# Kernel tuning notes

Hardware: AMD Instinct MI355X
Metric: run time of the kernel (lower is better)

## Reference

```python
import jax, jax.numpy as jnp
import numpy as np

B, S, H = 4, 512, 128

def setup_inputs() -> dict:
    key = jax.random.key(0)
    ks = jax.random.split(key, 6)
    scale = 1.0 / np.sqrt(2 * H)
    return {
        "query": jax.random.normal(ks[0], (B, S, H), dtype=jnp.float32),
        "key": jax.random.normal(ks[1], (B, S, H), dtype=jnp.float32),
        "value": jax.random.normal(ks[2], (B, S, H), dtype=jnp.float32),
        "attn_W": jax.random.normal(ks[3], (H, 2 * H), dtype=jnp.float32) * scale,  # torch Linear weight [out=H, in=2H]
        "attn_b": jax.random.normal(ks[4], (H,), dtype=jnp.float32) * scale,
        "v_w": jax.random.normal(ks[5], (1, H), dtype=jnp.float32) * (1.0 / np.sqrt(H)),
    }

def reference(query, key, value, attn_W, attn_b, v_w):
    # Split the concat-linear into query/key halves: cat([q,k]) @ W.T == q @ Wq.T + k @ Wk.T
    Wq = attn_W[:, :H]  # [H, H]
    Wk = attn_W[:, H:]  # [H, H]
    q_proj = jnp.einsum('bsh,oh->bso', query, Wq) + attn_b  # [B,S,H]
    k_proj = jnp.einsum('bth,oh->bto', key, Wk)             # [B,S,H]
    # tanh(q_proj[:, :, None] + k_proj[:, None, :]) -> [B,S,S,H]
    hidden = jnp.tanh(q_proj[:, :, None, :] + k_proj[:, None, :, :])
    scores = jnp.einsum('bsth,h->bst', hidden, v_w[0])      # [B,S,S]
    attention_weights = jax.nn.softmax(scores, axis=-1)
    # dropout is identity in eval mode
    output = jnp.einsum('bst,bth->bsh', attention_weights, value)
    return output, attention_weights
```

## Files before the change

### kernel.cpp

```cpp
#include <hip/hip_runtime.h>

#define Bn 4
#define Sn 512
#define Hn 128
#define ST 4

__device__ __forceinline__ float fast_exp2(float x) { return __builtin_amdgcn_exp2f(x); }
__device__ __forceinline__ float fast_rcp(float x)  { return __builtin_amdgcn_rcpf(x); }

#define C2 2.8853900817779268f

__global__ __launch_bounds__(256) void proj_kernel(
    const float* __restrict__ query, const float* __restrict__ key,
    const float* __restrict__ attn_W, const float* __restrict__ attn_b,
    float* __restrict__ eq, float* __restrict__ ekT)
{
    __shared__ float rows[2][4][Hn];
    const int row0 = blockIdx.x * 4;
    const int b    = row0 / Sn;
    const int t0   = row0 % Sn;
    const int tid  = threadIdx.x;

    {
        int src = tid >> 7, r = (tid >> 5) & 3, c4 = tid & 31;
        ((float4*)rows)[tid] =
            reinterpret_cast<const float4*>(src ? key : query)[(row0 + r) * 32 + c4];
    }
    __syncthreads();

    const int o     = tid & 127;
    const int which = tid >> 7;
    float acc[4] = {0,0,0,0};
    const float* wrow = attn_W + o * (2 * Hn) + which * Hn;
    for (int c = 0; c < Hn; c += 4) {
        float4 wv = *reinterpret_cast<const float4*>(wrow + c);
        #pragma unroll
        for (int r = 0; r < 4; r++) {
            float4 rv = *reinterpret_cast<const float4*>(&rows[which][r][c]);
            acc[r] += rv.x * wv.x + rv.y * wv.y + rv.z * wv.z + rv.w * wv.w;
        }
    }
    if (which == 0) {
        float bias = attn_b[o];
        #pragma unroll
        for (int r = 0; r < 4; r++)
            eq[(row0 + r) * Hn + o] = fast_exp2(C2 * (acc[r] + bias));
    } else {
        float4 ev;
        ev.x = fast_exp2(C2 * acc[0]); ev.y = fast_exp2(C2 * acc[1]);
        ev.z = fast_exp2(C2 * acc[2]); ev.w = fast_exp2(C2 * acc[3]);
        *reinterpret_cast<float4*>(&ekT[(size_t)(b * Hn + o) * Sn + t0]) = ev;
    }
}

__global__ __launch_bounds__(256) void score_kernel(
    const float* __restrict__ eq, const float* __restrict__ ekT,
    const float* __restrict__ v_w, float* __restrict__ logits)
{
    const int b  = blockIdx.y;
    const int s  = blockIdx.x * ST + (threadIdx.x >> 6);
    const int t0 = blockIdx.z * 256 + (threadIdx.x & 63) * 4;

    const float* kb   = ekT + (size_t)b * Hn * Sn + t0;
    const float* qrow = eq + (size_t)(b * Sn + s) * Hn;

    float a0 = 0.f, a1 = 0.f, a2 = 0.f, a3 = 0.f;
    for (int h = 0; h < Hn; h += 8) {
        float4 qA = *reinterpret_cast<const float4*>(qrow + h);
        float4 qB = *reinterpret_cast<const float4*>(qrow + h + 4);
        float4 wA = *reinterpret_cast<const float4*>(v_w + h);
        float4 wB = *reinterpret_cast<const float4*>(v_w + h + 4);
        const float qj[8] = {qA.x, qA.y, qA.z, qA.w, qB.x, qB.y, qB.z, qB.w};
        const float wj[8] = {wA.x, wA.y, wA.z, wA.w, wB.x, wB.y, wB.z, wB.w};
        #pragma unroll
        for (int j = 0; j < 8; j++) {
            float4 e = *reinterpret_cast<const float4*>(kb + (size_t)(h + j) * Sn);
            const float q = qj[j], w = wj[j];
            a0 += w * fast_rcp(q * e.x + 1.0f);
            a1 += w * fast_rcp(q * e.y + 1.0f);
            a2 += w * fast_rcp(q * e.z + 1.0f);
            a3 += w * fast_rcp(q * e.w + 1.0f);
        }
    }
    float4 o;
    o.x = -2.0f * a0; o.y = -2.0f * a1; o.z = -2.0f * a2; o.w = -2.0f * a3;
    *reinterpret_cast<float4*>(logits + (size_t)(b * Sn + s) * Sn + t0) = o;
}

__global__ __launch_bounds__(512) void softpv_kernel(
    const float* __restrict__ value, float* __restrict__ out,
    float* __restrict__ out_w)
{
    __shared__ float4 scT4[Sn];
    __shared__ float4 part4[16][ST][Hn / 4];

    const int b   = blockIdx.y;
    const int s0  = blockIdx.x * ST;
    const int tid = threadIdx.x;
    const int wave = tid >> 6, lane = tid & 63;

    if (wave < ST) {
        const int sr = wave;
        float* row = out_w + (size_t)(b * Sn + s0 + sr) * Sn;
        float v[8]; float m = -1e30f;
        #pragma unroll
        for (int i = 0; i < 8; i++) { v[i] = row[lane + i * 64]; m = fmaxf(m, v[i]); }
        #pragma unroll
        for (int off = 32; off; off >>= 1) m = fmaxf(m, __shfl_xor(m, off, 64));
        float sum = 0.f;
        const float l2e = 1.4426950408889634f;
        #pragma unroll
        for (int i = 0; i < 8; i++) { v[i] = fast_exp2((v[i] - m) * l2e); sum += v[i]; }
        #pragma unroll
        for (int off = 32; off; off >>= 1) sum += __shfl_xor(sum, off, 64);
        float inv = 1.0f / sum;
        #pragma unroll
        for (int i = 0; i < 8; i++) {
            float wgt = v[i] * inv;
            row[lane + i * 64] = wgt;
            ((float*)&scT4[lane + i * 64])[sr] = wgt;
        }
    }
    __syncthreads();

    {
        const int hq = tid & 31, tg = tid >> 5;
        const float* vb = value + ((size_t)b * Sn + tg * 32) * Hn + hq * 4;
        float4 A0 = {0,0,0,0}, A1 = {0,0,0,0}, A2 = {0,0,0,0}, A3 = {0,0,0,0};
        #pragma unroll 4
        for (int i = 0; i < 32; i++) {
            float4 v4 = *reinterpret_cast<const float4*>(vb + i * Hn);
            float4 w4 = scT4[tg * 32 + i];
            A0.x += w4.x * v4.x; A0.y += w4.x * v4.y; A0.z += w4.x * v4.z; A0.w += w4.x * v4.w;
            A1.x += w4.y * v4.x; A1.y += w4.y * v4.y; A1.z += w4.y * v4.z; A1.w += w4.y * v4.w;
            A2.x += w4.z * v4.x; A2.y += w4.z * v4.y; A2.z += w4.z * v4.z; A2.w += w4.z * v4.w;
            A3.x += w4.w * v4.x; A3.y += w4.w * v4.y; A3.z += w4.w * v4.z; A3.w += w4.w * v4.w;
        }
        part4[tg][0][hq] = A0;
        part4[tg][1][hq] = A1;
        part4[tg][2][hq] = A2;
        part4[tg][3][hq] = A3;
    }
    __syncthreads();
    {
        const int sg = tid >> 7, h = tid & 127;
        float r = 0.f;
        #pragma unroll
        for (int tg = 0; tg < 16; tg++)
            r += ((const float*)&part4[tg][sg][h >> 2])[h & 3];
        out[(b * Sn + s0 + sg) * Hn + h] = r;
    }
}

extern "C" void kernel_launch(void* const* d_in, const int* in_sizes, int n_in,
                              void* d_out, int out_size, void* d_ws, size_t ws_size,
                              hipStream_t stream) {
    const float* query  = (const float*)d_in[0];
    const float* key    = (const float*)d_in[1];
    const float* value  = (const float*)d_in[2];
    const float* attn_W = (const float*)d_in[3];
    const float* attn_b = (const float*)d_in[4];
    const float* v_w    = (const float*)d_in[5];

    float* out   = (float*)d_out;
    float* out_w = out + Bn * Sn * Hn;

    float* eq  = (float*)d_ws;
    float* ekT = eq + Bn * Sn * Hn;

    proj_kernel<<<Bn * Sn / 4, 256, 0, stream>>>(query, key, attn_W, attn_b, eq, ekT);
    score_kernel<<<dim3(Sn / ST, Bn, 2), 256, 0, stream>>>(eq, ekT, v_w, out_w);
    softpv_kernel<<<dim3(Sn / ST, Bn), 512, 0, stream>>>(value, out, out_w);
}
```

Baseline: 45.31 us.

## Register-tile score kernel over 4x4 outputs and split hidden dim into partial logits

The score kernel now computes a 4x4 (query rows by key columns) tile per thread. It stages query values and v_w in shared memory and software-prefetches the next ekT row, so each loaded key value is reused across four query rows. The hidden dimension is split into two halves across blocks. Each half writes partial logits to a workspace buffer, and the softmax kernel adds them back together. This cuts global load traffic per reciprocal and adds grid parallelism, at the cost of an extra partial-logit buffer write and read.

```diff
diff --git a/kernel.cpp b/kernel.cpp
--- a/kernel.cpp
+++ b/kernel.cpp
@@ -55,41 +55,76 @@
 
 __global__ __launch_bounds__(256) void score_kernel(
     const float* __restrict__ eq, const float* __restrict__ ekT,
-    const float* __restrict__ v_w, float* __restrict__ logits)
+    const float* __restrict__ v_w, float* __restrict__ pl)
 {
-    const int b  = blockIdx.y;
-    const int s  = blockIdx.x * ST + (threadIdx.x >> 6);
-    const int t0 = blockIdx.z * 256 + (threadIdx.x & 63) * 4;
-
-    const float* kb   = ekT + (size_t)b * Hn * Sn + t0;
-    const float* qrow = eq + (size_t)(b * Sn + s) * Hn;
-
-    float a0 = 0.f, a1 = 0.f, a2 = 0.f, a3 = 0.f;
-    for (int h = 0; h < Hn; h += 8) {
-        float4 qA = *reinterpret_cast<const float4*>(qrow + h);
-        float4 qB = *reinterpret_cast<const float4*>(qrow + h + 4);
-        float4 wA = *reinterpret_cast<const float4*>(v_w + h);
-        float4 wB = *reinterpret_cast<const float4*>(v_w + h + 4);
-        const float qj[8] = {qA.x, qA.y, qA.z, qA.w, qB.x, qB.y, qB.z, qB.w};
-        const float wj[8] = {wA.x, wA.y, wA.z, wA.w, wB.x, wB.y, wB.z, wB.w};
-        #pragma unroll
-        for (int j = 0; j < 8; j++) {
-            float4 e = *reinterpret_cast<const float4*>(kb + (size_t)(h + j) * Sn);
-            const float q = qj[j], w = wj[j];
-            a0 += w * fast_rcp(q * e.x + 1.0f);
-            a1 += w * fast_rcp(q * e.y + 1.0f);
-            a2 += w * fast_rcp(q * e.z + 1.0f);
-            a3 += w * fast_rcp(q * e.w + 1.0f);
-        }
-    }
-    float4 o;
-    o.x = -2.0f * a0; o.y = -2.0f * a1; o.z = -2.0f * a2; o.w = -2.0f * a3;
-    *reinterpret_cast<float4*>(logits + (size_t)(b * Sn + s) * Sn + t0) = o;
+    __shared__ float4 qs[8][64];
+    __shared__ float  ws[64];
+
+    const int b   = blockIdx.y;
+    const int s0b = blockIdx.x * 32;
+    const int tq  = blockIdx.z >> 1;
+    const int hh  = blockIdx.z & 1;
+    const int hb  = hh * 64;
+    const int tid = threadIdx.x;
+    const int tc  = tid & 31;
+    const int sg  = tid >> 5;
+    const int t0  = tq * 128 + tc * 4;
+
+    for (int i = tid; i < 2048; i += 256) {
+        int isg = i >> 8, sl = (i >> 6) & 3, h = i & 63;
+        ((float*)&qs[isg][h])[sl] =
+            eq[(size_t)(b * Sn + s0b + isg * 4 + sl) * Hn + hb + h];
+    }
+    if (tid < 64) ws[tid] = v_w[hb + tid];
+    __syncthreads();
+
+    const float* kb = ekT + ((size_t)b * Hn + hb) * Sn + t0;
+    float4 A0 = {0,0,0,0}, A1 = {0,0,0,0}, A2 = {0,0,0,0}, A3 = {0,0,0,0};
+
+    float4 cur = *reinterpret_cast<const float4*>(kb);
+    #pragma unroll 4
+    for (int h = 0; h < 63; h++) {
+        float4 nxt = *reinterpret_cast<const float4*>(kb + (size_t)(h + 1) * Sn);
+        float4 q4 = qs[sg][h];
+        float  w  = ws[h];
+        A0.x += w * fast_rcp(q4.x * cur.x + 1.f); A0.y += w * fast_rcp(q4.x * cur.y + 1.f);
+        A0.z += w * fast_rcp(q4.x * cur.z + 1.f); A0.w += w * fast_rcp(q4.x * cur.w + 1.f);
+        A1.x += w * fast_rcp(q4.y * cur.x + 1.f); A1.y += w * fast_rcp(q4.y * cur.y + 1.f);
+        A1.z += w * fast_rcp(q4.y * cur.z + 1.f); A1.w += w * fast_rcp(q4.y * cur.w + 1.f);
+        A2.x += w * fast_rcp(q4.z * cur.x + 1.f); A2.y += w * fast_rcp(q4.z * cur.y + 1.f);
+        A2.z += w * fast_rcp(q4.z * cur.z + 1.f); A2.w += w * fast_rcp(q4.z * cur.w + 1.f);
+        A3.x += w * fast_rcp(q4.w * cur.x + 1.f); A3.y += w * fast_rcp(q4.w * cur.y + 1.f);
+        A3.z += w * fast_rcp(q4.w * cur.z + 1.f); A3.w += w * fast_rcp(q4.w * cur.w + 1.f);
+        cur = nxt;
+    }
+    {
+        float4 q4 = qs[sg][63];
+        float  w  = ws[63];
+        A0.x += w * fast_rcp(q4.x * cur.x + 1.f); A0.y += w * fast_rcp(q4.x * cur.y + 1.f);
+        A0.z += w * fast_rcp(q4.x * cur.z + 1.f); A0.w += w * fast_rcp(q4.x * cur.w + 1.f);
+        A1.x += w * fast_rcp(q4.y * cur.x + 1.f); A1.y += w * fast_rcp(q4.y * cur.y + 1.f);
+        A1.z += w * fast_rcp(q4.y * cur.z + 1.f); A1.w += w * fast_rcp(q4.y * cur.w + 1.f);
+        A2.x += w * fast_rcp(q4.z * cur.x + 1.f); A2.y += w * fast_rcp(q4.z * cur.y + 1.f);
+        A2.z += w * fast_rcp(q4.z * cur.z + 1.f); A2.w += w * fast_rcp(q4.z * cur.w + 1.f);
+        A3.x += w * fast_rcp(q4.w * cur.x + 1.f); A3.y += w * fast_rcp(q4.w * cur.y + 1.f);
+        A3.z += w * fast_rcp(q4.w * cur.z + 1.f); A3.w += w * fast_rcp(q4.w * cur.w + 1.f);
+    }
+
+    float* dst = pl + (((size_t)hh * Bn + b) * Sn + (s0b + sg * 4)) * Sn + t0;
+    float4 O;
+    O.x = -2.f * A0.x; O.y = -2.f * A0.y; O.z = -2.f * A0.z; O.w = -2.f * A0.w;
+    *reinterpret_cast<float4*>(dst)           = O;
+    O.x = -2.f * A1.x; O.y = -2.f * A1.y; O.z = -2.f * A1.z; O.w = -2.f * A1.w;
+    *reinterpret_cast<float4*>(dst + Sn)      = O;
+    O.x = -2.f * A2.x; O.y = -2.f * A2.y; O.z = -2.f * A2.z; O.w = -2.f * A2.w;
+    *reinterpret_cast<float4*>(dst + 2 * Sn)  = O;
+    O.x = -2.f * A3.x; O.y = -2.f * A3.y; O.z = -2.f * A3.z; O.w = -2.f * A3.w;
+    *reinterpret_cast<float4*>(dst + 3 * Sn)  = O;
 }
 
 __global__ __launch_bounds__(512) void softpv_kernel(
-    const float* __restrict__ value, float* __restrict__ out,
-    float* __restrict__ out_w)
+    const float* __restrict__ value, const float* __restrict__ pl,
+    float* __restrict__ out, float* __restrict__ out_w)
 {
     __shared__ float4 scT4[Sn];
     __shared__ float4 part4[16][ST][Hn / 4];
@@ -101,10 +136,14 @@
 
     if (wave < ST) {
         const int sr = wave;
-        float* row = out_w + (size_t)(b * Sn + s0 + sr) * Sn;
+        const float* r0 = pl + ((size_t)(0 * Bn + b) * Sn + (s0 + sr)) * Sn;
+        const float* r1 = pl + ((size_t)(1 * Bn + b) * Sn + (s0 + sr)) * Sn;
         float v[8]; float m = -1e30f;
         #pragma unroll
-        for (int i = 0; i < 8; i++) { v[i] = row[lane + i * 64]; m = fmaxf(m, v[i]); }
+        for (int i = 0; i < 8; i++) {
+            v[i] = r0[lane + i * 64] + r1[lane + i * 64];
+            m = fmaxf(m, v[i]);
+        }
         #pragma unroll
         for (int off = 32; off; off >>= 1) m = fmaxf(m, __shfl_xor(m, off, 64));
         float sum = 0.f;
@@ -114,10 +153,11 @@
         #pragma unroll
         for (int off = 32; off; off >>= 1) sum += __shfl_xor(sum, off, 64);
         float inv = 1.0f / sum;
+        float* wrow_out = out_w + (size_t)(b * Sn + s0 + sr) * Sn;
         #pragma unroll
         for (int i = 0; i < 8; i++) {
             float wgt = v[i] * inv;
-            row[lane + i * 64] = wgt;
+            wrow_out[lane + i * 64] = wgt;
             ((float*)&scT4[lane + i * 64])[sr] = wgt;
         }
     }
@@ -167,8 +207,9 @@
 
     float* eq  = (float*)d_ws;
     float* ekT = eq + Bn * Sn * Hn;
+    float* pl  = ekT + Bn * Hn * Sn;
 
     proj_kernel<<<Bn * Sn / 4, 256, 0, stream>>>(query, key, attn_W, attn_b, eq, ekT);
-    score_kernel<<<dim3(Sn / ST, Bn, 2), 256, 0, stream>>>(eq, ekT, v_w, out_w);
-    softpv_kernel<<<dim3(Sn / ST, Bn), 512, 0, stream>>>(value, out, out_w);
-}
+    score_kernel<<<dim3(16, Bn, 8), 256, 0, stream>>>(eq, ekT, v_w, pl);
+    softpv_kernel<<<dim3(Sn / ST, Bn), 512, 0, stream>>>(value, pl, out, out_w);
+}
```

Result: slower. 47.13 us (+4.0%).
